# Optimization experiments

Measured on AMD Instinct MI355X. Metric: run time of the kernel, lower is better.

Reference implementation:

```python
import jax, jax.numpy as jnp
import numpy as np

N = 100_000        # num nodes
E = 1_600_000      # num edges (avg degree 16)
F_IN = 128         # input node feature dim
F_E = 32           # edge feature dim
D = 32             # out_dim per head
H = 4              # heads


def setup_inputs() -> dict:
    key = jax.random.key(0)
    ks = jax.random.split(key, 8)
    s = 0.05
    return {
        "node_features": jax.random.normal(ks[0], (N, F_IN), jnp.float32),
        "edge_index": jax.random.randint(ks[1], (E, 2), 0, N, jnp.int32),
        "edge_features": jax.random.normal(ks[2], (E, F_E), jnp.float32),
        "W_node": jax.random.normal(ks[3], (F_IN, D * H), jnp.float32) * s,
        "W_edge": jax.random.normal(ks[4], (F_E, D * H), jnp.float32) * s,
        "attn_kernel": jax.random.normal(ks[5], (H, 3 * D), jnp.float32) * s,
        "W_out": jax.random.normal(ks[6], (D * H, D), jnp.float32) * s,
        "b_out": jnp.zeros((D,), jnp.float32),
    }


def segment_softmax(logits, seg, num_segments):
    # logits: [E, H], seg: [E] destination node ids
    mx = jax.ops.segment_max(logits, seg, num_segments=num_segments)   # [N, H]
    ex = jnp.exp(logits - mx[seg])
    denom = jax.ops.segment_sum(ex, seg, num_segments=num_segments)    # [N, H]
    return ex / (denom[seg] + 1e-8)


def reference(node_features, edge_index, edge_features, W_node, W_edge,
              attn_kernel, W_out, b_out):
    src_idx = edge_index[:, 0]
    dst_idx = edge_index[:, 1]

    # Node / edge projections -> [*, H, D]
    node_proj = (node_features @ W_node).reshape(N, H, D)
    edge_proj = (edge_features @ W_edge).reshape(E, H, D)

    # attn_kernel is [H, 3D] applied to concat(src, dst, edge); split it so we
    # never materialize the [E, H, 3D] concat. Src/dst terms are computed
    # per-node then gathered (same math, far less traffic).
    a_src, a_dst, a_edge = attn_kernel[:, :D], attn_kernel[:, D:2 * D], attn_kernel[:, 2 * D:]
    s_src = jnp.einsum('nhd,hd->nh', node_proj, a_src)   # [N, H]
    s_dst = jnp.einsum('nhd,hd->nh', node_proj, a_dst)   # [N, H]
    s_edge = jnp.einsum('ehd,hd->eh', edge_proj, a_edge)  # [E, H]

    logits = s_src[src_idx] + s_dst[dst_idx] + s_edge     # [E, H]
    attn = segment_softmax(logits, dst_idx, N)             # [E, H]

    src_feat = node_proj[src_idx]                          # [E, H, D]
    messages = (attn[:, :, None] * src_feat).reshape(E, H * D)
    agg = jax.ops.segment_sum(messages, dst_idx, num_segments=N)  # [N, H*D]

    out = jax.nn.gelu(agg @ W_out + b_out, approximate=False)     # exact erf GELU
    return out
```

## Files before the change

kernel.cpp:

```cpp
#include <hip/hip_runtime.h>
#include <hip/hip_bf16.h>
#include <hip/hip_fp16.h>

#define F_IN 128
#define F_E  32
#define DH   128
#define HD   32

__device__ __forceinline__ unsigned short f2bf(float f) {
    unsigned int x = __float_as_uint(f);
    unsigned int r = (x + 0x7fffu + ((x >> 16) & 1u)) >> 16;
    return (unsigned short)r;
}

__global__ void prep_kernel(const float* __restrict__ W_edge,
                            const float* __restrict__ attn,
                            float* __restrict__ wefold) {
    int t = threadIdx.x;
    int f = t >> 2, h = t & 3;
    float s = 0.f;
#pragma unroll
    for (int d = 0; d < 32; ++d)
        s += W_edge[f * DH + h * HD + d] * attn[h * 96 + 64 + d];
    wefold[f * 4 + h] = s;
}

__global__ __launch_bounds__(256, 4)
void node_proj_kernel(const float* __restrict__ x, const float* __restrict__ Wn,
                      const float* __restrict__ attn,
                      unsigned short* __restrict__ proj_bf,
                      float* __restrict__ s_src, int N) {
    __shared__ float xsT[32 * 132];
    __shared__ float ws[32 * 132];
    const int t  = threadIdx.x;
    const int n0 = blockIdx.x * 128;
    const int tc = t & 15, tn = t >> 4;
    const float4* x4  = (const float4*)x;
    const float4* Wn4 = (const float4*)Wn;

    float acc[2][2][4][4];
#pragma unroll
    for (int a = 0; a < 2; ++a)
#pragma unroll
        for (int b = 0; b < 2; ++b)
#pragma unroll
            for (int i = 0; i < 4; ++i)
#pragma unroll
                for (int j = 0; j < 4; ++j) acc[a][b][i][j] = 0.f;

    for (int ch = 0; ch < 4; ++ch) {
        __syncthreads();
#pragma unroll
        for (int j = 0; j < 4; ++j) {
            int idx = t + j * 256;
            int n  = idx >> 3;
            int kq = idx & 7;
            float4 v = make_float4(0.f, 0.f, 0.f, 0.f);
            if (n0 + n < N) v = x4[(size_t)(n0 + n) * 32 + ch * 8 + kq];
            int kk = kq * 4;
            xsT[(kk + 0) * 132 + n] = v.x;
            xsT[(kk + 1) * 132 + n] = v.y;
            xsT[(kk + 2) * 132 + n] = v.z;
            xsT[(kk + 3) * 132 + n] = v.w;
        }
#pragma unroll
        for (int j = 0; j < 4; ++j) {
            int idx = t + j * 256;
            int kk = idx >> 5, cq = idx & 31;
            float4 v = Wn4[(size_t)(ch * 32 + kk) * 32 + cq];
            *(float4*)&ws[kk * 132 + cq * 4] = v;
        }
        __syncthreads();
#pragma unroll 4
        for (int kk = 0; kk < 32; ++kk) {
            float4 a0 = *(const float4*)&xsT[kk * 132 + tn * 4];
            float4 a1 = *(const float4*)&xsT[kk * 132 + 64 + tn * 4];
            float4 b0 = *(const float4*)&ws[kk * 132 + tc * 4];
            float4 b1 = *(const float4*)&ws[kk * 132 + 64 + tc * 4];
            float av[2][4] = {{a0.x, a0.y, a0.z, a0.w}, {a1.x, a1.y, a1.z, a1.w}};
            float bv[2][4] = {{b0.x, b0.y, b0.z, b0.w}, {b1.x, b1.y, b1.z, b1.w}};
#pragma unroll
            for (int ni = 0; ni < 2; ++ni)
#pragma unroll
                for (int ci = 0; ci < 2; ++ci)
#pragma unroll
                    for (int ii = 0; ii < 4; ++ii)
#pragma unroll
                        for (int jj = 0; jj < 4; ++jj)
                            acc[ni][ci][ii][jj] =
                                fmaf(av[ni][ii], bv[ci][jj], acc[ni][ci][ii][jj]);
        }
    }

    float asv[2][4];
#pragma unroll
    for (int ci = 0; ci < 2; ++ci)
#pragma unroll
        for (int jj = 0; jj < 4; ++jj) {
            int c = ci * 64 + tc * 4 + jj;
            int h = c >> 5, d = c & 31;
            asv[ci][jj] = attn[h * 96 + d];
        }

#pragma unroll
    for (int ni = 0; ni < 2; ++ni)
#pragma unroll
        for (int ii = 0; ii < 4; ++ii) {
            int n = n0 + ni * 64 + tn * 4 + ii;
            bool ok = (n < N);
            if (ok) {
                union { unsigned short h[4]; uint2 u; } p0, p1;
#pragma unroll
                for (int jj = 0; jj < 4; ++jj) {
                    p0.h[jj] = f2bf(acc[ni][0][ii][jj]);
                    p1.h[jj] = f2bf(acc[ni][1][ii][jj]);
                }
                *(uint2*)&proj_bf[(size_t)n * DH + tc * 4]      = p0.u;
                *(uint2*)&proj_bf[(size_t)n * DH + 64 + tc * 4] = p1.u;
            }
#pragma unroll
            for (int ci = 0; ci < 2; ++ci) {
                float ps = 0.f;
#pragma unroll
                for (int jj = 0; jj < 4; ++jj)
                    ps = fmaf(acc[ni][ci][ii][jj], asv[ci][jj], ps);
                ps += __shfl_xor(ps, 1);
                ps += __shfl_xor(ps, 2);
                ps += __shfl_xor(ps, 4);
                if (ok && (tc & 7) == 0) {
                    int h = ci * 2 + (tc >> 3);
                    s_src[n * 4 + h] = ps;
                }
            }
        }
}

__global__ __launch_bounds__(256)
void edgeprep_kernel(const float* __restrict__ ef, const int* __restrict__ eidx,
                     const float* __restrict__ wefold,
                     const float* __restrict__ s_src,
                     int* __restrict__ cnt, uint4* __restrict__ rec_e, int E) {
    __shared__ float wf[128];
    const int t = threadIdx.x;
    if (t < 128) wf[t] = wefold[t];
    __syncthreads();

    const int e = blockIdx.x * 256 + t;
    if (e >= E) return;
    int2 sd = ((const int2*)eidx)[e];
    int s_i = sd.x, d_i = sd.y;
    float es0 = 0.f, es1 = 0.f, es2 = 0.f, es3 = 0.f;
#pragma unroll
    for (int f4 = 0; f4 < 8; ++f4) {
        float4 v = *(const float4*)&ef[(size_t)e * F_E + f4 * 4];
        float vv[4] = {v.x, v.y, v.z, v.w};
#pragma unroll
        for (int q = 0; q < 4; ++q) {
            float4 wv = *(const float4*)&wf[(f4 * 4 + q) * 4];
            es0 = fmaf(vv[q], wv.x, es0);
            es1 = fmaf(vv[q], wv.y, es1);
            es2 = fmaf(vv[q], wv.z, es2);
            es3 = fmaf(vv[q], wv.w, es3);
        }
    }
    float4 a = *(const float4*)&s_src[s_i * 4];
    float w0 = __expf(a.x + es0), w1 = __expf(a.y + es1);
    float w2 = __expf(a.z + es2), w3 = __expf(a.w + es3);
    unsigned int u0 = __half_as_ushort(__float2half_rn(w0));
    unsigned int u1 = __half_as_ushort(__float2half_rn(w1));
    unsigned int u2 = __half_as_ushort(__float2half_rn(w2));
    unsigned int u3 = __half_as_ushort(__float2half_rn(w3));
    int r = atomicAdd(&cnt[d_i], 1);
    uint4 R;
    R.x = (unsigned int)s_i;
    R.y = u0 | (u1 << 16);
    R.z = u2 | (u3 << 16);
    R.w = ((unsigned int)d_i << 15) | (unsigned int)r;
    rec_e[e] = R;
}

__global__ __launch_bounds__(256)
void scan1_kernel(const int* __restrict__ cnt, int* __restrict__ cursor,
                  int* __restrict__ bsum, int N) {
    __shared__ int s[256];
    const int t = threadIdx.x;
    int i = blockIdx.x * 256 + t;
    int v = (i < N) ? cnt[i] : 0;
    s[t] = v;
    __syncthreads();
#pragma unroll
    for (int d = 1; d < 256; d <<= 1) {
        int x = (t >= d) ? s[t - d] : 0;
        __syncthreads();
        s[t] += x;
        __syncthreads();
    }
    if (i < N) cursor[i] = s[t] - v;
    if (t == 255) bsum[blockIdx.x] = s[255];
}

__global__ __launch_bounds__(512)
void scan2_kernel(int* __restrict__ bsum, int nb) {
    __shared__ int s[512];
    const int t = threadIdx.x;
    int v = (t < nb) ? bsum[t] : 0;
    s[t] = v;
    __syncthreads();
#pragma unroll
    for (int d = 1; d < 512; d <<= 1) {
        int x = (t >= d) ? s[t - d] : 0;
        __syncthreads();
        s[t] += x;
        __syncthreads();
    }
    if (t < nb) bsum[t] = s[t] - v;
}

__global__ __launch_bounds__(256)
void scatter_kernel(const uint4* __restrict__ rec_e,
                    const int* __restrict__ cursor,
                    const int* __restrict__ bsum,
                    uint4* __restrict__ rec, int E) {
    const int e = blockIdx.x * 256 + threadIdx.x;
    if (e >= E) return;
    uint4 R = rec_e[e];
    int d = (int)(R.w >> 15);
    int r = (int)(R.w & 32767u);
    int pos = cursor[d] + bsum[d >> 8] + r;
    rec[pos] = R;
}

__global__ __launch_bounds__(256)
void gather_kernel(const int* __restrict__ cursor, const int* __restrict__ bsum,
                   const uint4* __restrict__ rec,
                   const unsigned int* __restrict__ proj_bf,
                   unsigned int* __restrict__ numer_bf, int N, int E) {
    const int t    = threadIdx.x;
    const int lane = t & 63;
    const int n    = blockIdx.x * 4 + (t >> 6);
    if (n >= N) return;

    int start = cursor[n] + bsum[n >> 8];
    int end   = (n == N - 1) ? E : (cursor[n + 1] + bsum[(n + 1) >> 8]);
    start = __builtin_amdgcn_readfirstlane(start);
    end   = __builtin_amdgcn_readfirstlane(end);

    const int  hf  = lane >> 5;
    const int  col = lane & 31;
    const int  h   = col >> 3;
    const bool hiw = (h & 1) != 0;
    const bool low = (h < 2);

    float4 acc = make_float4(0.f, 0.f, 0.f, 0.f);
    float dsum = 0.f;

    auto SEL = [&](uint4 qa, uint4 qb, int j, int cc,
                   unsigned int& sx, unsigned int& wp) {
        unsigned int s  = hf ? qb.x : qa.x;
        unsigned int py = hf ? qb.y : qa.y;
        unsigned int pz = hf ? qb.z : qa.z;
        bool v = (2 * j + hf) < cc;
        sx = v ? s : 0u;
        unsigned int pk = low ? py : pz;
        wp = v ? pk : 0u;
    };
    auto FMA = [&](unsigned int wp, uint2 pv) {
        unsigned short uw = hiw ? (unsigned short)(wp >> 16)
                                : (unsigned short)(wp & 0xffffu);
        float w = __half2float(__ushort_as_half(uw));
        dsum += w;
        acc.x = fmaf(w, __uint_as_float(pv.x << 16), acc.x);
        acc.y = fmaf(w, __uint_as_float(pv.x & 0xffff0000u), acc.y);
        acc.z = fmaf(w, __uint_as_float(pv.y << 16), acc.z);
        acc.w = fmaf(w, __uint_as_float(pv.y & 0xffff0000u), acc.w);
    };

    int i   = start;
    int rem = end - start;
    int c0  = rem < 8 ? rem : 8;

    unsigned int sx0, sx1, sx2, sx3, wp0, wp1, wp2, wp3;
    {
        uint4 q0 = rec[i + 0], q1 = rec[i + 1], q2 = rec[i + 2], q3 = rec[i + 3];
        uint4 q4 = rec[i + 4], q5 = rec[i + 5], q6 = rec[i + 6], q7 = rec[i + 7];
        SEL(q0, q1, 0, c0, sx0, wp0);
        SEL(q2, q3, 1, c0, sx1, wp1);
        SEL(q4, q5, 2, c0, sx2, wp2);
        SEL(q6, q7, 3, c0, sx3, wp3);
    }

    while (c0 > 0) {
        const int i1   = i + c0;
        const int rem1 = rem - c0;
        const int c1   = rem1 < 8 ? rem1 : 8;
        uint4 q0 = rec[i1 + 0], q1 = rec[i1 + 1], q2 = rec[i1 + 2], q3 = rec[i1 + 3];
        uint4 q4 = rec[i1 + 4], q5 = rec[i1 + 5], q6 = rec[i1 + 6], q7 = rec[i1 + 7];
        uint2 pv0 = *(const uint2*)&proj_bf[(size_t)sx0 * 64 + col * 2];
        uint2 pv1 = *(const uint2*)&proj_bf[(size_t)sx1 * 64 + col * 2];
        uint2 pv2 = *(const uint2*)&proj_bf[(size_t)sx2 * 64 + col * 2];
        uint2 pv3 = *(const uint2*)&proj_bf[(size_t)sx3 * 64 + col * 2];
        FMA(wp0, pv0);
        FMA(wp1, pv1);
        FMA(wp2, pv2);
        FMA(wp3, pv3);
        SEL(q0, q1, 0, c1, sx0, wp0);
        SEL(q2, q3, 1, c1, sx1, wp1);
        SEL(q4, q5, 2, c1, sx2, wp2);
        SEL(q6, q7, 3, c1, sx3, wp3);
        i = i1; rem = rem1; c0 = c1;
    }

    dsum  += __shfl_xor(dsum, 32);
    acc.x += __shfl_xor(acc.x, 32);
    acc.y += __shfl_xor(acc.y, 32);
    acc.z += __shfl_xor(acc.z, 32);
    acc.w += __shfl_xor(acc.w, 32);

    if (hf == 0) {
        float r = 1.f / (dsum + 1e-8f);
        uint2 p;
        p.x = (unsigned int)f2bf(acc.x * r) | ((unsigned int)f2bf(acc.y * r) << 16);
        p.y = (unsigned int)f2bf(acc.z * r) | ((unsigned int)f2bf(acc.w * r) << 16);
        *(uint2*)&numer_bf[(size_t)n * 64 + col * 2] = p;
    }
}

__global__ __launch_bounds__(256, 2)
void out_kernel(const unsigned int* __restrict__ numer_bf,
                const float* __restrict__ Wout, const float* __restrict__ bout,
                float* __restrict__ out, int N) {
    __shared__ float wsh[128 * 32];
    __shared__ float bsh[32];
    const int t = threadIdx.x;
    for (int i = t; i < 4096; i += 256) wsh[i] = Wout[i];
    if (t < 32) bsh[t] = bout[t];
    __syncthreads();

    int n = blockIdx.x * 256 + t;
    if (n >= N) return;

    float acc[32];
#pragma unroll
    for (int j = 0; j < 32; ++j) acc[j] = 0.f;

    for (int kg = 0; kg < 16; ++kg) {
        uint4 v = *(const uint4*)&numer_bf[(size_t)n * 64 + kg * 4];
        unsigned int vv[4] = {v.x, v.y, v.z, v.w};
#pragma unroll
        for (int q = 0; q < 4; ++q) {
            int k = kg * 8 + q * 2;
            float a0 = __uint_as_float(vv[q] << 16);
            float a1 = __uint_as_float(vv[q] & 0xffff0000u);
#pragma unroll
            for (int j = 0; j < 32; j += 4) {
                float4 w0 = *(const float4*)&wsh[k * 32 + j];
                float4 w1 = *(const float4*)&wsh[(k + 1) * 32 + j];
                acc[j + 0] = fmaf(a0, w0.x, fmaf(a1, w1.x, acc[j + 0]));
                acc[j + 1] = fmaf(a0, w0.y, fmaf(a1, w1.y, acc[j + 1]));
                acc[j + 2] = fmaf(a0, w0.z, fmaf(a1, w1.z, acc[j + 2]));
                acc[j + 3] = fmaf(a0, w0.w, fmaf(a1, w1.w, acc[j + 3]));
            }
        }
    }
#pragma unroll
    for (int j = 0; j < 32; ++j) {
        float z = acc[j] + bsh[j];
        acc[j] = 0.5f * z * (1.f + erff(z * 0.70710678118654752f));
    }
#pragma unroll
    for (int j = 0; j < 32; j += 4)
        *(float4*)&out[(size_t)n * 32 + j] = make_float4(acc[j], acc[j+1], acc[j+2], acc[j+3]);
}

extern "C" void kernel_launch(void* const* d_in, const int* in_sizes, int n_in,
                              void* d_out, int out_size, void* d_ws, size_t ws_size,
                              hipStream_t stream) {
    const float* x    = (const float*)d_in[0];
    const int*   eidx = (const int*)d_in[1];
    const float* ef   = (const float*)d_in[2];
    const float* Wn   = (const float*)d_in[3];
    const float* We   = (const float*)d_in[4];
    const float* attn = (const float*)d_in[5];
    const float* Wout = (const float*)d_in[6];
    const float* bout = (const float*)d_in[7];
    float* out = (float*)d_out;

    const int N = in_sizes[0] / F_IN;
    const int E = in_sizes[1] / 2;
    const int NB = (N + 255) / 256;

    char* ws = (char*)d_ws;
    size_t off = 0;
    auto alloc = [&](size_t bytes) {
        void* p = ws + off;
        off = (off + bytes + 255) & ~(size_t)255;
        return p;
    };
    int*   cnt     = (int*)  alloc((size_t)N * 4);
    size_t zero_bytes = off;
    int*   cursor  = (int*)  alloc((size_t)N * 4);
    int*   bsum    = (int*)  alloc(512 * 4);
    float* wefold  = (float*)alloc(512);
    float* s_src   = (float*)alloc((size_t)N * 4 * 4);
    unsigned short* proj_bf = (unsigned short*)alloc((size_t)N * DH * 2);
    size_t numer_bytes = (size_t)N * 64 * 4;
    size_t rece_bytes  = (size_t)E * 16;
    unsigned int* numer_bf = (unsigned int*)alloc(numer_bytes > rece_bytes ?
                                                  numer_bytes : rece_bytes);
    uint4* rec_e   = (uint4*)numer_bf;
    uint4* rec     = (uint4*)alloc((size_t)E * 16 + 128);

    hipMemsetAsync(d_ws, 0, zero_bytes, stream);
    hipLaunchKernelGGL(prep_kernel, dim3(1), dim3(128), 0, stream, We, attn, wefold);
    hipLaunchKernelGGL(node_proj_kernel, dim3((N + 127) / 128), dim3(256), 0, stream,
                       x, Wn, attn, proj_bf, s_src, N);
    hipLaunchKernelGGL(edgeprep_kernel, dim3((E + 255) / 256), dim3(256), 0, stream,
                       ef, eidx, wefold, s_src, cnt, rec_e, E);
    hipLaunchKernelGGL(scan1_kernel, dim3(NB), dim3(256), 0, stream, cnt, cursor, bsum, N);
    hipLaunchKernelGGL(scan2_kernel, dim3(1), dim3(512), 0, stream, bsum, NB);
    hipLaunchKernelGGL(scatter_kernel, dim3((E + 255) / 256), dim3(256), 0, stream,
                       rec_e, cursor, bsum, rec, E);
    hipLaunchKernelGGL(gather_kernel, dim3((N + 3) / 4), dim3(256), 0, stream,
                       cursor, bsum, rec, (const unsigned int*)proj_bf, numer_bf, N, E);
    hipLaunchKernelGGL(out_kernel, dim3((N + 255) / 256), dim3(256), 0, stream,
                       numer_bf, Wout, bout, out, N);
}
```

Before: 522.6 us.

## Compute node projection with bf16 MFMA instead of fp32 FMA

Rewrites the node projection GEMM so it uses bf16 MFMA 16x16x32 instructions on XOR-swizzled shared-memory tiles of the full 128-wide K dimension, rather than a scalar fp32 outer-product loop. The per-head s_src reduction is adapted to the MFMA output layout, and the bf16 projection is staged through shared memory so global stores are coalesced. This trades fp32 precision on the inputs for bf16 and uses 64KB of LDS with lower occupancy. The node projection is only one of several kernels in the pipeline, so the effect on total time may be limited.

```diff
diff --git a/kernel.cpp b/kernel.cpp
--- a/kernel.cpp
+++ b/kernel.cpp
@@ -6,6 +6,9 @@
 #define F_E  32
 #define DH   128
 #define HD   32
+
+using bf16x8 = __attribute__((ext_vector_type(8))) short;
+using f32x4  = __attribute__((ext_vector_type(4))) float;
 
 __device__ __forceinline__ unsigned short f2bf(float f) {
     unsigned int x = __float_as_uint(f);
@@ -25,114 +28,134 @@
     wefold[f * 4 + h] = s;
 }
 
-__global__ __launch_bounds__(256, 4)
+__global__ __launch_bounds__(256, 2)
 void node_proj_kernel(const float* __restrict__ x, const float* __restrict__ Wn,
                       const float* __restrict__ attn,
                       unsigned short* __restrict__ proj_bf,
                       float* __restrict__ s_src, int N) {
-    __shared__ float xsT[32 * 132];
-    __shared__ float ws[32 * 132];
-    const int t  = threadIdx.x;
-    const int n0 = blockIdx.x * 128;
-    const int tc = t & 15, tn = t >> 4;
-    const float4* x4  = (const float4*)x;
-    const float4* Wn4 = (const float4*)Wn;
-
-    float acc[2][2][4][4];
-#pragma unroll
-    for (int a = 0; a < 2; ++a)
-#pragma unroll
-        for (int b = 0; b < 2; ++b)
-#pragma unroll
-            for (int i = 0; i < 4; ++i)
-#pragma unroll
-                for (int j = 0; j < 4; ++j) acc[a][b][i][j] = 0.f;
-
-    for (int ch = 0; ch < 4; ++ch) {
-        __syncthreads();
+    __shared__ __align__(16) unsigned char xb[32768];
+    __shared__ __align__(16) unsigned char wb[32768];
+    const int t    = threadIdx.x;
+    const int n0   = blockIdx.x * 128;
+    const int lane = t & 63;
+    const int wid  = t >> 6;
+    const int lg   = lane >> 4;
+    const int lm   = lane & 15;
+
+    {
+        const float4* x4 = (const float4*)x;
+#pragma unroll
+        for (int j = 0; j < 16; ++j) {
+            int idx = t + j * 256;
+            int n   = idx >> 5;
+            int kq  = idx & 31;
+            float4 v = make_float4(0.f, 0.f, 0.f, 0.f);
+            if (n0 + n < N) v = x4[(size_t)(n0 + n) * 32 + kq];
+            unsigned int lo = (unsigned int)f2bf(v.x) | ((unsigned int)f2bf(v.y) << 16);
+            unsigned int hi = (unsigned int)f2bf(v.z) | ((unsigned int)f2bf(v.w) << 16);
+            int byte = (n * 256 + kq * 8) ^ ((n & 7) << 4);
+            *(uint2*)&xb[byte] = make_uint2(lo, hi);
+        }
+    }
+    {
+        const int c  = t & 127;
+        const int kg = t >> 7;
+#pragma unroll
+        for (int jb = 0; jb < 8; ++jb) {
+            int k0 = kg * 64 + jb * 8;
+            unsigned int p0, p1, p2, p3;
+            {
+                float a0 = Wn[(size_t)(k0 + 0) * 128 + c];
+                float a1 = Wn[(size_t)(k0 + 1) * 128 + c];
+                float a2 = Wn[(size_t)(k0 + 2) * 128 + c];
+                float a3 = Wn[(size_t)(k0 + 3) * 128 + c];
+                float a4 = Wn[(size_t)(k0 + 4) * 128 + c];
+                float a5 = Wn[(size_t)(k0 + 5) * 128 + c];
+                float a6 = Wn[(size_t)(k0 + 6) * 128 + c];
+                float a7 = Wn[(size_t)(k0 + 7) * 128 + c];
+                p0 = (unsigned int)f2bf(a0) | ((unsigned int)f2bf(a1) << 16);
+                p1 = (unsigned int)f2bf(a2) | ((unsigned int)f2bf(a3) << 16);
+                p2 = (unsigned int)f2bf(a4) | ((unsigned int)f2bf(a5) << 16);
+                p3 = (unsigned int)f2bf(a6) | ((unsigned int)f2bf(a7) << 16);
+            }
+            int byte = (c * 256 + k0 * 2) ^ ((c & 7) << 4);
+            *(uint4*)&wb[byte] = make_uint4(p0, p1, p2, p3);
+        }
+    }
+    __syncthreads();
+
+    const int wrow = wid * 32;
+    f32x4 acc[2][8];
+#pragma unroll
+    for (int fm = 0; fm < 2; ++fm)
+#pragma unroll
+        for (int fn = 0; fn < 8; ++fn)
+#pragma unroll
+            for (int q = 0; q < 4; ++q) acc[fm][fn][q] = 0.f;
+
+#pragma unroll
+    for (int ks = 0; ks < 4; ++ks) {
+        bf16x8 bfr[8];
+#pragma unroll
+        for (int fn = 0; fn < 8; ++fn) {
+            int col  = fn * 16 + lm;
+            int byte = (col * 256 + ks * 64 + lg * 16) ^ ((col & 7) << 4);
+            bfr[fn] = *(const bf16x8*)&wb[byte];
+        }
+#pragma unroll
+        for (int fm = 0; fm < 2; ++fm) {
+            int row  = wrow + fm * 16 + lm;
+            int byte = (row * 256 + ks * 64 + lg * 16) ^ ((row & 7) << 4);
+            bf16x8 afr = *(const bf16x8*)&xb[byte];
+#pragma unroll
+            for (int fn = 0; fn < 8; ++fn)
+                acc[fm][fn] = __builtin_amdgcn_mfma_f32_16x16x32_bf16(
+                    afr, bfr[fn], acc[fm][fn], 0, 0, 0);
+        }
+    }
+
+    float asv[8];
+#pragma unroll
+    for (int fn = 0; fn < 8; ++fn)
+        asv[fn] = attn[(fn >> 1) * 96 + (fn & 1) * 16 + lm];
+#pragma unroll
+    for (int fm = 0; fm < 2; ++fm)
 #pragma unroll
         for (int j = 0; j < 4; ++j) {
-            int idx = t + j * 256;
-            int n  = idx >> 3;
-            int kq = idx & 7;
-            float4 v = make_float4(0.f, 0.f, 0.f, 0.f);
-            if (n0 + n < N) v = x4[(size_t)(n0 + n) * 32 + ch * 8 + kq];
-            int kk = kq * 4;
-            xsT[(kk + 0) * 132 + n] = v.x;
-            xsT[(kk + 1) * 132 + n] = v.y;
-            xsT[(kk + 2) * 132 + n] = v.z;
-            xsT[(kk + 3) * 132 + n] = v.w;
-        }
-#pragma unroll
-        for (int j = 0; j < 4; ++j) {
-            int idx = t + j * 256;
-            int kk = idx >> 5, cq = idx & 31;
-            float4 v = Wn4[(size_t)(ch * 32 + kk) * 32 + cq];
-            *(float4*)&ws[kk * 132 + cq * 4] = v;
-        }
-        __syncthreads();
-#pragma unroll 4
-        for (int kk = 0; kk < 32; ++kk) {
-            float4 a0 = *(const float4*)&xsT[kk * 132 + tn * 4];
-            float4 a1 = *(const float4*)&xsT[kk * 132 + 64 + tn * 4];
-            float4 b0 = *(const float4*)&ws[kk * 132 + tc * 4];
-            float4 b1 = *(const float4*)&ws[kk * 132 + 64 + tc * 4];
-            float av[2][4] = {{a0.x, a0.y, a0.z, a0.w}, {a1.x, a1.y, a1.z, a1.w}};
-            float bv[2][4] = {{b0.x, b0.y, b0.z, b0.w}, {b1.x, b1.y, b1.z, b1.w}};
-#pragma unroll
-            for (int ni = 0; ni < 2; ++ni)
-#pragma unroll
-                for (int ci = 0; ci < 2; ++ci)
-#pragma unroll
-                    for (int ii = 0; ii < 4; ++ii)
-#pragma unroll
-                        for (int jj = 0; jj < 4; ++jj)
-                            acc[ni][ci][ii][jj] =
-                                fmaf(av[ni][ii], bv[ci][jj], acc[ni][ci][ii][jj]);
-        }
-    }
-
-    float asv[2][4];
-#pragma unroll
-    for (int ci = 0; ci < 2; ++ci)
-#pragma unroll
-        for (int jj = 0; jj < 4; ++jj) {
-            int c = ci * 64 + tc * 4 + jj;
-            int h = c >> 5, d = c & 31;
-            asv[ci][jj] = attn[h * 96 + d];
-        }
-
-#pragma unroll
-    for (int ni = 0; ni < 2; ++ni)
-#pragma unroll
-        for (int ii = 0; ii < 4; ++ii) {
-            int n = n0 + ni * 64 + tn * 4 + ii;
-            bool ok = (n < N);
-            if (ok) {
-                union { unsigned short h[4]; uint2 u; } p0, p1;
-#pragma unroll
-                for (int jj = 0; jj < 4; ++jj) {
-                    p0.h[jj] = f2bf(acc[ni][0][ii][jj]);
-                    p1.h[jj] = f2bf(acc[ni][1][ii][jj]);
-                }
-                *(uint2*)&proj_bf[(size_t)n * DH + tc * 4]      = p0.u;
-                *(uint2*)&proj_bf[(size_t)n * DH + 64 + tc * 4] = p1.u;
-            }
-#pragma unroll
-            for (int ci = 0; ci < 2; ++ci) {
-                float ps = 0.f;
-#pragma unroll
-                for (int jj = 0; jj < 4; ++jj)
-                    ps = fmaf(acc[ni][ci][ii][jj], asv[ci][jj], ps);
+            int row = n0 + wrow + fm * 16 + lg * 4 + j;
+#pragma unroll
+            for (int h = 0; h < 4; ++h) {
+                float ps = fmaf(acc[fm][2 * h][j], asv[2 * h],
+                                acc[fm][2 * h + 1][j] * asv[2 * h + 1]);
                 ps += __shfl_xor(ps, 1);
                 ps += __shfl_xor(ps, 2);
                 ps += __shfl_xor(ps, 4);
-                if (ok && (tc & 7) == 0) {
-                    int h = ci * 2 + (tc >> 3);
-                    s_src[n * 4 + h] = ps;
-                }
+                ps += __shfl_xor(ps, 8);
+                if (lm == h && row < N) s_src[row * 4 + h] = ps;
             }
         }
+
+    __syncthreads();
+#pragma unroll
+    for (int fm = 0; fm < 2; ++fm)
+#pragma unroll
+        for (int fn = 0; fn < 8; ++fn)
+#pragma unroll
+            for (int j = 0; j < 4; ++j) {
+                int r = wrow + fm * 16 + lg * 4 + j;
+                int c = fn * 16 + lm;
+                *(unsigned short*)&xb[r * 256 + c * 2] = f2bf(acc[fm][fn][j]);
+            }
+    __syncthreads();
+#pragma unroll
+    for (int j = 0; j < 8; ++j) {
+        int idx = t + j * 256;
+        int row = idx >> 4;
+        if (n0 + row < N) {
+            uint4 v = *(const uint4*)&xb[idx * 16];
+            *(uint4*)&proj_bf[(size_t)(n0 + row) * 128 + (idx & 15) * 8] = v;
+        }
+    }
 }
 
 __global__ __launch_bounds__(256)
```

Measured after the change: 512.2 us. 2.0% less time.
